# Kernel optimization log

Hardware: AMD Instinct MI355X
Metric: run time of the kernel (lower is better)

The kernel has to match this reference:

```python
import jax, jax.numpy as jnp
import numpy as np

D = 768; NH = 12; HD = D // NH; L = 12; NC = 27; PATCH = 16; MLP = 3072; PROJ = 512
IMG = 224; GRID = IMG // PATCH; HW = GRID * GRID; S = NC + HW
NEG = -1e9

def _ln(x, w, b):
    m = jnp.mean(x, -1, keepdims=True)
    v = jnp.mean(jnp.square(x - m), -1, keepdims=True)
    return (x - m) * jax.lax.rsqrt(v + 1e-5) * w + b

def _quick_gelu(x):
    return x * jax.nn.sigmoid(1.702 * x)

def _build_mask(attn_obj_masks, dtype):
    # CRIS block mask: cls<->cls blocked except self; cls->patch allowed only for
    # patches of that class; patch->cls blocked; patch->patch fully allowed.
    B = attn_obj_masks.shape[0]
    oh = jax.nn.one_hot(attn_obj_masks, NC, dtype=dtype)              # [B, HW, NC]
    T11 = jnp.broadcast_to(1.0 - jnp.eye(NC, dtype=dtype), (B, NC, NC))
    M13 = 1.0 - jnp.swapaxes(oh, 1, 2)                                # [B, NC, HW]
    top = jnp.concatenate([T11, M13], axis=2)
    bot = jnp.concatenate([jnp.ones((B, HW, NC), dtype), jnp.zeros((B, HW, HW), dtype)], axis=2)
    Mb = jnp.concatenate([top, bot], axis=1)                          # [B, S, S]
    return jnp.where(Mb == 1.0, jnp.asarray(NEG, dtype), jnp.asarray(0.0, dtype))

def reference(img, sents, attn_obj_masks, obj_masks, cls_tokens, patch_w, patch_b, pos_embed,
              ln1_w, ln1_b, qkv_w, qkv_b, out_w, out_b, ln2_w, ln2_b,
              mlp_w1, mlp_b1, mlp_w2, mlp_b2, ln_post_w, ln_post_b, proj):
    B = img.shape[0]
    sents = sents / jnp.linalg.norm(sents, axis=-1, keepdims=True)    # encode_text output, L2 normed
    mask = _build_mask(attn_obj_masks, img.dtype)                     # [B, S, S]
    # patch embedding (conv stride 16) -> [B, HW, D]
    p = jax.lax.conv_general_dilated(img, patch_w, (PATCH, PATCH), 'VALID',
                                     dimension_numbers=('NCHW', 'OIHW', 'NCHW'))
    p = p.reshape(B, D, HW).transpose(0, 2, 1) + patch_b
    x = jnp.concatenate([jnp.broadcast_to(cls_tokens, (B, NC, D)), p], axis=1) + pos_embed
    scale = 1.0 / np.sqrt(HD).astype(np.float32)
    def block(x, prm):
        l1w, l1b, qw, qb, ow, ob, l2w, l2b, w1, b1, w2, b2 = prm
        h = _ln(x, l1w, l1b)
        qkv = h @ qw + qb
        q, k, v = jnp.split(qkv, 3, axis=-1)
        q = q.reshape(B, S, NH, HD).transpose(0, 2, 1, 3)
        k = k.reshape(B, S, NH, HD).transpose(0, 2, 1, 3)
        v = v.reshape(B, S, NH, HD).transpose(0, 2, 1, 3)
        scores = jnp.einsum('bhqd,bhkd->bhqk', q, k) * scale + mask[:, None]
        a = jax.nn.softmax(scores, axis=-1)
        o = jnp.einsum('bhqk,bhkd->bhqd', a, v).transpose(0, 2, 1, 3).reshape(B, S, D)
        x = x + o @ ow + ob
        h = _ln(x, l2w, l2b)
        x = x + _quick_gelu(h @ w1 + b1) @ w2 + b2
        return x, None
    x, _ = jax.lax.scan(block, x, (ln1_w, ln1_b, qkv_w, qkv_b, out_w, out_b,
                                   ln2_w, ln2_b, mlp_w1, mlp_b1, mlp_w2, mlp_b2))
    tokens = _ln(x, ln_post_w, ln_post_b) @ proj                      # [B, S, PROJ]
    obj = tokens[:, :NC]
    obj = obj / jnp.linalg.norm(obj, axis=-1, keepdims=True)
    pred_id = jnp.einsum('bnd,bd->bn', obj, sents)                    # [B, NC]
    # per-class scatter loop == gather of pred_id by per-pixel class id
    pred = jnp.take_along_axis(pred_id, obj_masks.reshape(B, -1), axis=1).reshape(obj_masks.shape)
    return pred                                                       # [B, 224, 224]

def setup_inputs():
    B = 16; std = 0.02
    ks = jax.random.split(jax.random.key(0), 16)
    f = jax.random.normal
    return {
        'img': f(ks[0], (B, 3, IMG, IMG), jnp.float32),
        'sents': f(ks[1], (B, PROJ), jnp.float32),
        'attn_obj_masks': jax.random.randint(ks[2], (B, HW), 0, NC, jnp.int32),
        'obj_masks': jax.random.randint(ks[3], (B, IMG, IMG), 0, NC, jnp.int32),
        'cls_tokens': f(ks[4], (1, NC, D)) * std,
        'patch_w': f(ks[5], (D, 3, PATCH, PATCH)) * std,
        'patch_b': jnp.zeros((D,)),
        'pos_embed': f(ks[6], (S, D)) * std,
        'ln1_w': jnp.ones((L, D)), 'ln1_b': jnp.zeros((L, D)),
        'qkv_w': f(ks[7], (L, D, 3 * D)) * std, 'qkv_b': jnp.zeros((L, 3 * D)),
        'out_w': f(ks[8], (L, D, D)) * std, 'out_b': jnp.zeros((L, D)),
        'ln2_w': jnp.ones((L, D)), 'ln2_b': jnp.zeros((L, D)),
        'mlp_w1': f(ks[9], (L, D, MLP)) * std, 'mlp_b1': jnp.zeros((L, MLP)),
        'mlp_w2': f(ks[10], (L, MLP, D)) * std, 'mlp_b2': jnp.zeros((L, D)),
        'ln_post_w': jnp.ones((D,)), 'ln_post_b': jnp.zeros((D,)),
        'proj': f(ks[11], (D, PROJ)) * std,
    }
```

## Files before the change

kernel.cpp:

```cpp
#include <hip/hip_runtime.h>

#define DEV __device__ __forceinline__

typedef short bf16x8 __attribute__((ext_vector_type(8)));
typedef float f32x4 __attribute__((ext_vector_type(4)));
typedef int vi4 __attribute__((ext_vector_type(4)));
typedef unsigned uint2v __attribute__((ext_vector_type(2)));
typedef unsigned short u16;
typedef short short4v __attribute__((ext_vector_type(4)));

#define NEGV -1000000000.0f

DEV u16 f2bf(float f) {
  union { float f; unsigned u; } v; v.f = f;
  unsigned r = v.u + 0x7FFFu + ((v.u >> 16) & 1u);
  return (u16)(r >> 16);
}

DEV bf16x8 ld_bf8(const u16* p) {
  vi4 v = *(const vi4*)p;
  return __builtin_bit_cast(bf16x8, v);
}

DEV void gload_lds16(const u16* g, vi4* l) {
  __builtin_amdgcn_global_load_lds((const __attribute__((address_space(1))) void*)g,
                                   (__attribute__((address_space(3))) void*)l, 16, 0, 0);
}

DEV unsigned lds_off(const void* p) {
  return (unsigned)(unsigned long long)(const __attribute__((address_space(3))) void*)p;
}

DEV uint2v ds_tr16(unsigned byteaddr) {
  uint2v r;
  asm volatile("ds_read_b64_tr_b16 %0, %1" : "=v"(r) : "v"(byteaddr));
  return r;
}

template<int BN, int MODE, bool GELU, int KS>
__global__ __launch_bounds__(256) void gemm_bt(
    const u16* __restrict__ A, const u16* __restrict__ Bt,
    const float* __restrict__ bias,
    float* __restrict__ Cf, u16* __restrict__ Cb,
    int M, int N, int K, const float* __restrict__ pos, long pstride)
{
  constexpr int FJ = BN / 32;
  constexpr int LTOT = 4 + FJ;
  __shared__ vi4 As[2][1024];
  __shared__ vi4 Bs[2][BN * 8];

  int gx = gridDim.x, gy = gridDim.y;
  int nwg = gx * gy * (int)gridDim.z;
  int orig = blockIdx.x + gx * (blockIdx.y + gy * blockIdx.z);
  int qq = nwg >> 3, rr = nwg & 7;
  int xcd = orig & 7, off = orig >> 3;
  int id = (xcd < rr) ? xcd * (qq + 1) + off : rr * (qq + 1) + (xcd - rr) * qq + off;
  int bx = id % gx, rest = id / gx, by = rest % gy, bz = rest / gy;

  int tid = threadIdx.x, lane = tid & 63, wid = tid >> 6;
  int wm = wid >> 1, wn = wid & 1;
  int m0 = by * 128, n0 = bx * BN;
  int kBeg = (K / KS) * bz;
  int nT = (K / KS) >> 6;
  f32x4 acc[4][FJ] = {};

  auto STAGE = [&](int buf, int kk) {
    #pragma unroll
    for (int r = 0; r < 4; ++r) {
      int flat = r * 256 + tid;
      int row = flat >> 3, c = flat & 7;
      int cs = c ^ (row & 7);
      gload_lds16(A + (long)(m0 + row) * K + kk + cs * 8, &As[buf][r * 256 + wid * 64]);
    }
    #pragma unroll
    for (int r = 0; r < FJ; ++r) {
      int flat = r * 256 + tid;
      int row = flat >> 3, c = flat & 7;
      int cs = c ^ (row & 7);
      gload_lds16(Bt + (long)(n0 + row) * K + kk + cs * 8, &Bs[buf][r * 256 + wid * 64]);
    }
  };

  STAGE(0, kBeg);
  int cur = 0;
  for (int t = 0; t < nT; ++t) {
    if (t + 1 < nT) {
      STAGE(cur ^ 1, kBeg + (t + 1) * 64);
      asm volatile("s_waitcnt vmcnt(%0)" :: "i"(LTOT) : "memory");
    } else {
      asm volatile("s_waitcnt vmcnt(0)" ::: "memory");
    }
    __builtin_amdgcn_s_barrier();
    int cg = lane >> 4, l15 = lane & 15;
    #pragma unroll
    for (int ks = 0; ks < 2; ++ks) {
      bf16x8 af[4], bfr[FJ];
      #pragma unroll
      for (int i = 0; i < 4; ++i) {
        int ra = wm * 64 + i * 16 + l15;
        af[i] = __builtin_bit_cast(bf16x8, As[cur][ra * 8 + ((ks * 4 + cg) ^ (ra & 7))]);
      }
      #pragma unroll
      for (int j = 0; j < FJ; ++j) {
        int rb = wn * (BN / 2) + j * 16 + l15;
        bfr[j] = __builtin_bit_cast(bf16x8, Bs[cur][rb * 8 + ((ks * 4 + cg) ^ (rb & 7))]);
      }
      #pragma unroll
      for (int i = 0; i < 4; ++i)
        #pragma unroll
        for (int j = 0; j < FJ; ++j)
          acc[i][j] = __builtin_amdgcn_mfma_f32_16x16x32_bf16(af[i], bfr[j], acc[i][j], 0, 0, 0);
    }
    __builtin_amdgcn_s_barrier();
    cur ^= 1;
  }

  int cg = lane >> 4, l15 = lane & 15;
  float* Cfz = (MODE == 2 && KS > 1) ? Cf + (long)bz * pstride : Cf;
  #pragma unroll
  for (int i = 0; i < 4; ++i) {
    #pragma unroll
    for (int j = 0; j < FJ; ++j) {
      int col = n0 + wn * (BN / 2) + j * 16 + l15;
      float bv = bias ? bias[col] : 0.f;
      #pragma unroll
      for (int r = 0; r < 4; ++r) {
        int row = m0 + wm * 64 + i * 16 + cg * 4 + r;
        if (row < M) {
          float v = acc[i][j][r];
          if (KS == 1 || bz == 0) v += bv;
          if (GELU) v = v / (1.f + __expf(-1.702f * v));
          if (MODE == 0) Cb[(long)row * N + col] = f2bf(v);
          else if (MODE == 2) Cfz[(long)row * N + col] = v;
          else {
            int hw = row % 196;
            int xr = (row / 196) * 223 + 27 + hw;
            Cf[(long)xr * 768 + col] = v + pos[(27 + hw) * 768 + col];
          }
        }
      }
    }
  }
}

__global__ __launch_bounds__(256) void attn_kernel(
    const u16* __restrict__ QKV, const int* __restrict__ aom, u16* __restrict__ O)
{
  __shared__ vi4 Kl[224 * 8];
  __shared__ vi4 Vl[224 * 8];
  __shared__ int ml[196];
  int tid = threadIdx.x, lane = tid & 63, wid = tid >> 6;
  int orig = blockIdx.x + 2 * (blockIdx.y + 12 * blockIdx.z);
  int id = (orig & 7) * 48 + (orig >> 3);
  int qg = id & 1, h = (id >> 1) % 12, b = id / 24;
  long rowbase = (long)b * 223;
  #pragma unroll
  for (int it = 0; it < 7; ++it) {
    int flat = it * 256 + tid;
    int s = flat >> 3, c = flat & 7;
    int cs = c ^ (s & 7);
    gload_lds16(QKV + (rowbase + s) * 2304 + 768 + h * 64 + cs * 8, &Kl[it * 256 + wid * 64]);
  }
  #pragma unroll
  for (int it = 0; it < 7; ++it) {
    int u = it * 256 + tid;
    int slin = u >> 3, inner = u & 7;
    int sk = slin >> 2, sdp = slin & 3;
    int s = sk * 4 + (inner >> 1);
    int c = ((sdp ^ (sk & 3)) << 1) | (inner & 1);
    gload_lds16(QKV + (rowbase + s) * 2304 + 1536 + h * 64 + c * 8, &Vl[it * 256 + wid * 64]);
  }
  for (int i = tid; i < 196; i += 256) ml[i] = aom[b * 196 + i];
  __syncthreads();

  int l15 = lane & 15, cg = lane >> 4;
  unsigned vbase = lds_off(Vl);
  #pragma unroll
  for (int rep = 0; rep < 2; ++rep) {
    int fo = wid * 2 + rep;
    if (fo >= 7) break;
    int qf = qg * 7 + fo;
    int q0 = qf * 16;
    int arow = q0 + l15; if (arow > 222) arow = 222;
    const u16* qb = QKV + (rowbase + arow) * 2304 + h * 64;
    bf16x8 aq0 = ld_bf8(qb + cg * 8);
    bf16x8 aq1 = ld_bf8(qb + 32 + cg * 8);

    f32x4 sc[14];
    #pragma unroll
    for (int kf = 0; kf < 14; ++kf) {
      int key = kf * 16 + l15;
      f32x4 a = {0.f, 0.f, 0.f, 0.f};
      bf16x8 bk0 = __builtin_bit_cast(bf16x8, Kl[key * 8 + (cg ^ (key & 7))]);
      bf16x8 bk1 = __builtin_bit_cast(bf16x8, Kl[key * 8 + ((4 + cg) ^ (key & 7))]);
      a = __builtin_amdgcn_mfma_f32_16x16x32_bf16(bk0, aq0, a, 0, 0, 0);
      a = __builtin_amdgcn_mfma_f32_16x16x32_bf16(bk1, aq1, a, 0, 0, 0);
      sc[kf] = a;
    }
    int q = q0 + l15;
    float mx = -3.4e38f;
    #pragma unroll
    for (int kf = 0; kf < 14; ++kf) {
      #pragma unroll
      for (int r = 0; r < 4; ++r) {
        int key = kf * 16 + cg * 4 + r;
        float mval;
        if (key >= 223) mval = NEGV;
        else if (q >= 27) mval = (key < 27) ? NEGV : 0.f;
        else if (key < 27) mval = (key == q) ? 0.f : NEGV;
        else mval = (ml[key - 27] == q) ? 0.f : NEGV;
        float sv = sc[kf][r] * 0.125f + mval;
        sc[kf][r] = sv;
        mx = fmaxf(mx, sv);
      }
    }
    mx = fmaxf(mx, __shfl_xor(mx, 16));
    mx = fmaxf(mx, __shfl_xor(mx, 32));
    float sum = 0.f;
    #pragma unroll
    for (int kf = 0; kf < 14; ++kf) {
      #pragma unroll
      for (int r = 0; r < 4; ++r) {
        float e = __expf(sc[kf][r] - mx);
        sc[kf][r] = e; sum += e;
      }
    }
    sum += __shfl_xor(sum, 16);
    sum += __shfl_xor(sum, 32);
    float inv = 1.f / sum;
    unsigned plo[14], phi[14];
    #pragma unroll
    for (int kf = 0; kf < 14; ++kf) {
      plo[kf] = (unsigned)f2bf(sc[kf][0] * inv) | ((unsigned)f2bf(sc[kf][1] * inv) << 16);
      phi[kf] = (unsigned)f2bf(sc[kf][2] * inv) | ((unsigned)f2bf(sc[kf][3] * inv) << 16);
    }
    f32x4 oacc[4] = {};
    #pragma unroll
    for (int ks = 0; ks < 7; ++ks) {
      uint2v vr[4][2];
      int sk0 = ks * 8 + cg * 2, sk1 = sk0 + 1;
      #pragma unroll
      for (int nf = 0; nf < 4; ++nf) {
        vr[nf][0] = ds_tr16(vbase + (unsigned)(((sk0 * 4 + (nf ^ (sk0 & 3))) << 7) + l15 * 8));
        vr[nf][1] = ds_tr16(vbase + (unsigned)(((sk1 * 4 + (nf ^ (sk1 & 3))) << 7) + l15 * 8));
      }
      int src0 = ((cg & 1) << 5) + l15, src1 = src0 + 16;
      int lo0 = __shfl((int)plo[2 * ks], src0),     hi0 = __shfl((int)phi[2 * ks], src0);
      int lo1 = __shfl((int)plo[2 * ks + 1], src0), hi1 = __shfl((int)phi[2 * ks + 1], src0);
      int lo0b = __shfl((int)plo[2 * ks], src1),     hi0b = __shfl((int)phi[2 * ks], src1);
      int lo1b = __shfl((int)plo[2 * ks + 1], src1), hi1b = __shfl((int)phi[2 * ks + 1], src1);
      bool hg = (cg >> 1) & 1;
      vi4 paw = { hg ? lo1 : lo0, hg ? hi1 : hi0, hg ? lo1b : lo0b, hg ? hi1b : hi0b };
      bf16x8 pa = __builtin_bit_cast(bf16x8, paw);
      asm volatile("s_waitcnt lgkmcnt(0)" ::: "memory");
      __builtin_amdgcn_sched_barrier(0);
      #pragma unroll
      for (int nf = 0; nf < 4; ++nf) {
        vi4 bw = { (int)vr[nf][0][0], (int)vr[nf][0][1], (int)vr[nf][1][0], (int)vr[nf][1][1] };
        oacc[nf] = __builtin_amdgcn_mfma_f32_16x16x32_bf16(pa, __builtin_bit_cast(bf16x8, bw), oacc[nf], 0, 0, 0);
      }
    }
    #pragma unroll
    for (int nf = 0; nf < 4; ++nf) {
      int d = h * 64 + nf * 16 + l15;
      #pragma unroll
      for (int r = 0; r < 4; ++r) {
        int qo = q0 + cg * 4 + r;
        if (qo < 223) O[(rowbase + qo) * 768 + d] = f2bf(oacc[nf][r]);
      }
    }
  }
}

template<int NADD, bool MAP27, bool WRITEX>
__global__ __launch_bounds__(256) void ln_kernel(
    const float* __restrict__ X, const float* __restrict__ P, long ps,
    float* __restrict__ Xout, u16* __restrict__ Hb,
    const float* __restrict__ w, const float* __restrict__ bb, int nrows)
{
  int row = blockIdx.x * 4 + (threadIdx.x >> 6);
  if (row >= nrows) return;
  int xr = MAP27 ? (row / 27) * 223 + (row % 27) : row;
  int l = threadIdx.x & 63;
  const float4* xp = (const float4*)(X + (long)xr * 768);
  float4 a = xp[l], c = xp[l + 64], d = xp[l + 128];
  if (NADD == 2) {
    const float4* p0 = (const float4*)(P + (long)xr * 768);
    const float4* p1 = (const float4*)(P + ps + (long)xr * 768);
    float4 u0 = p0[l], u1 = p0[l + 64], u2 = p0[l + 128];
    float4 v0 = p1[l], v1 = p1[l + 64], v2 = p1[l + 128];
    a.x += u0.x + v0.x; a.y += u0.y + v0.y; a.z += u0.z + v0.z; a.w += u0.w + v0.w;
    c.x += u1.x + v1.x; c.y += u1.y + v1.y; c.z += u1.z + v1.z; c.w += u1.w + v1.w;
    d.x += u2.x + v2.x; d.y += u2.y + v2.y; d.z += u2.z + v2.z; d.w += u2.w + v2.w;
  }
  if (WRITEX) {
    float4* xo = (float4*)(Xout + (long)xr * 768);
    xo[l] = a; xo[l + 64] = c; xo[l + 128] = d;
  }
  float s = a.x + a.y + a.z + a.w + c.x + c.y + c.z + c.w + d.x + d.y + d.z + d.w;
  #pragma unroll
  for (int t = 1; t < 64; t <<= 1) s += __shfl_xor(s, t);
  float mean = s * (1.f / 768.f);
  a.x -= mean; a.y -= mean; a.z -= mean; a.w -= mean;
  c.x -= mean; c.y -= mean; c.z -= mean; c.w -= mean;
  d.x -= mean; d.y -= mean; d.z -= mean; d.w -= mean;
  float q = a.x*a.x + a.y*a.y + a.z*a.z + a.w*a.w
          + c.x*c.x + c.y*c.y + c.z*c.z + c.w*c.w
          + d.x*d.x + d.y*d.y + d.z*d.z + d.w*d.w;
  #pragma unroll
  for (int t = 1; t < 64; t <<= 1) q += __shfl_xor(q, t);
  float rs = rsqrtf(q * (1.f / 768.f) + 1e-5f);
  const float4* wp = (const float4*)w;
  const float4* bp = (const float4*)bb;
  u16* out = Hb + (long)row * 768;
  float4 w0 = wp[l], w1 = wp[l + 64], w2 = wp[l + 128];
  float4 b0 = bp[l], b1 = bp[l + 64], b2 = bp[l + 128];
  short4v o;
  o[0] = (short)f2bf(a.x * rs * w0.x + b0.x); o[1] = (short)f2bf(a.y * rs * w0.y + b0.y);
  o[2] = (short)f2bf(a.z * rs * w0.z + b0.z); o[3] = (short)f2bf(a.w * rs * w0.w + b0.w);
  *(short4v*)(out + l * 4) = o;
  o[0] = (short)f2bf(c.x * rs * w1.x + b1.x); o[1] = (short)f2bf(c.y * rs * w1.y + b1.y);
  o[2] = (short)f2bf(c.z * rs * w1.z + b1.z); o[3] = (short)f2bf(c.w * rs * w1.w + b1.w);
  *(short4v*)(out + 256 + l * 4) = o;
  o[0] = (short)f2bf(d.x * rs * w2.x + b2.x); o[1] = (short)f2bf(d.y * rs * w2.y + b2.y);
  o[2] = (short)f2bf(d.z * rs * w2.z + b2.z); o[3] = (short)f2bf(d.w * rs * w2.w + b2.w);
  *(short4v*)(out + 512 + l * 4) = o;
}

__global__ __launch_bounds__(256) void transpose_w(
    const float* __restrict__ W, u16* __restrict__ WT, int K, int N, long sW, long sT)
{
  __shared__ float t[64][65];
  int z = blockIdx.z;
  W += (long)z * sW; WT += (long)z * sT;
  int n0 = blockIdx.x * 64, k0 = blockIdx.y * 64;
  #pragma unroll
  for (int i = 0; i < 4; ++i) {
    int flat = i * 256 + threadIdx.x;
    int r = flat >> 4, c = (flat & 15) * 4;
    float4 v = *(const float4*)(W + (long)(k0 + r) * N + n0 + c);
    t[r][c] = v.x; t[r][c + 1] = v.y; t[r][c + 2] = v.z; t[r][c + 3] = v.w;
  }
  __syncthreads();
  #pragma unroll
  for (int i = 0; i < 8; ++i) {
    int flat = i * 256 + threadIdx.x;
    int rn = flat >> 5, ck = (flat & 31) * 2;
    unsigned val = (unsigned)f2bf(t[ck][rn]) | ((unsigned)f2bf(t[ck + 1][rn]) << 16);
    *(unsigned*)(WT + (long)(n0 + rn) * K + k0 + ck) = val;
  }
}

__global__ void convert_bf16(const float* __restrict__ src, u16* __restrict__ dst, int n) {
  int i = blockIdx.x * 256 + threadIdx.x;
  if (i < n) dst[i] = f2bf(src[i]);
}

__global__ __launch_bounds__(192) void patch_extract(const float* __restrict__ img, u16* __restrict__ Xp) {
  int row = blockIdx.x;
  int t = threadIdx.x;
  int pair = t >> 2, part = t & 3;
  int cch = pair >> 4, kh = pair & 15;
  int b = row / 196, hw = row % 196, gh = hw / 14, gw = hw % 14;
  float4 v = *(const float4*)(img + ((long)(b * 3 + cch) * 224 + gh * 16 + kh) * 224 + gw * 16 + part * 4);
  short4v o;
  o[0] = (short)f2bf(v.x); o[1] = (short)f2bf(v.y); o[2] = (short)f2bf(v.z); o[3] = (short)f2bf(v.w);
  *(short4v*)(Xp + (long)row * 768 + pair * 16 + part * 4) = o;
}

__global__ void cls_pos_fill(const float* __restrict__ cls, const float* __restrict__ pos, float* __restrict__ x) {
  int i = blockIdx.x * 256 + threadIdx.x;
  if (i >= 16 * 27 * 768) return;
  int d = i % 768, t = i / 768, b = t / 27, s = t % 27;
  x[((long)b * 223 + s) * 768 + d] = cls[s * 768 + d] + pos[s * 768 + d];
}

__global__ __launch_bounds__(256) void sents_norm(const float* __restrict__ s, float* __restrict__ sn) {
  __shared__ float sb[4];
  int b = blockIdx.x, t = threadIdx.x;
  float v0 = s[b * 512 + t], v1 = s[b * 512 + t + 256];
  float q = v0 * v0 + v1 * v1;
  #pragma unroll
  for (int d = 1; d < 64; d <<= 1) q += __shfl_xor(q, d);
  if ((t & 63) == 0) sb[t >> 6] = q;
  __syncthreads();
  float inv = rsqrtf(sb[0] + sb[1] + sb[2] + sb[3]);
  sn[b * 512 + t] = v0 * inv;
  sn[b * 512 + t + 256] = v1 * inv;
}

__global__ __launch_bounds__(256) void obj_dot(const float* __restrict__ obj, const float* __restrict__ sn, float* __restrict__ pid) {
  __shared__ float sb[8];
  int r = blockIdx.x, t = threadIdx.x, b = r / 27;
  float v0 = obj[(long)r * 512 + t], v1 = obj[(long)r * 512 + t + 256];
  float w0 = sn[b * 512 + t], w1 = sn[b * 512 + t + 256];
  float q = v0 * v0 + v1 * v1;
  float dt = v0 * w0 + v1 * w1;
  #pragma unroll
  for (int d = 1; d < 64; d <<= 1) { q += __shfl_xor(q, d); dt += __shfl_xor(dt, d); }
  if ((t & 63) == 0) { sb[t >> 6] = q; sb[4 + (t >> 6)] = dt; }
  __syncthreads();
  if (t == 0) pid[r] = (sb[4] + sb[5] + sb[6] + sb[7]) * rsqrtf(sb[0] + sb[1] + sb[2] + sb[3]);
}

__global__ void gather_pred(const int* __restrict__ om, const float* __restrict__ pid, float* __restrict__ out) {
  int i = blockIdx.x * 256 + threadIdx.x;
  if (i >= 16 * 224 * 224) return;
  int b = i / (224 * 224);
  out[i] = pid[b * 27 + om[i]];
}

extern "C" void kernel_launch(void* const* d_in, const int* in_sizes, int n_in,
                              void* d_out, int out_size, void* d_ws, size_t ws_size,
                              hipStream_t stream) {
  const float* img     = (const float*)d_in[0];
  const float* sents   = (const float*)d_in[1];
  const int*   aom     = (const int*)d_in[2];
  const int*   omask   = (const int*)d_in[3];
  const float* cls     = (const float*)d_in[4];
  const float* patch_w = (const float*)d_in[5];
  const float* patch_b = (const float*)d_in[6];
  const float* pos     = (const float*)d_in[7];
  const float* ln1w    = (const float*)d_in[8];
  const float* ln1b    = (const float*)d_in[9];
  const float* qkvw    = (const float*)d_in[10];
  const float* qkvb    = (const float*)d_in[11];
  const float* outw    = (const float*)d_in[12];
  const float* outb    = (const float*)d_in[13];
  const float* ln2w    = (const float*)d_in[14];
  const float* ln2b    = (const float*)d_in[15];
  const float* m1w     = (const float*)d_in[16];
  const float* m1b     = (const float*)d_in[17];
  const float* m2w     = (const float*)d_in[18];
  const float* m2b     = (const float*)d_in[19];
  const float* lnpw    = (const float*)d_in[20];
  const float* lnpb    = (const float*)d_in[21];
  const float* projw   = (const float*)d_in[22];

  char* p = (char*)d_ws;
  auto alloc = [&](size_t bytes) { char* r = p; p += (bytes + 255) & ~(size_t)255; return r; };
  const long PS = 3584l * 768;
  float* x   = (float*)alloc(3568ul * 768 * 4);
  u16* H     = (u16*)alloc(3584ul * 768 * 2);
  u16* QKV   = (u16*)alloc(3584ul * 2304 * 2);
  u16* Obuf  = (u16*)alloc(3584ul * 768 * 2);
  u16* G     = (u16*)alloc(3584ul * 3072 * 2);
  float* Y   = (float*)alloc((size_t)PS * 2 * 4);
  float* Mp  = (float*)alloc((size_t)PS * 2 * 4);
  u16* PWc   = (u16*)alloc(768ul * 768 * 2);
  u16* PrT   = (u16*)alloc(512ul * 768 * 2);
  float* obj = (float*)alloc(432ul * 512 * 4);
  float* sn  = (float*)alloc(16ul * 512 * 4);
  float* pid = (float*)alloc(432ul * 4);

  const size_t wlayer = (2304ul * 768 + 768ul * 768 + 3072ul * 768 + 768ul * 3072) * 2;
  size_t used = (size_t)(p - (char*)d_ws);
  int nw = (ws_size >= used + 12 * wlayer + 65536) ? 12 : 1;
  const long sQ = 2304l * 768, sO = 768l * 768, s1 = 768l * 3072, s2 = 3072l * 768;
  u16* WqT = (u16*)alloc((size_t)sQ * 2 * nw);
  u16* WoT = (u16*)alloc((size_t)sO * 2 * nw);
  u16* W1T = (u16*)alloc((size_t)s1 * 2 * nw);
  u16* W2T = (u16*)alloc((size_t)s2 * 2 * nw);

  convert_bf16<<<2304, 256, 0, stream>>>(patch_w, PWc, 768 * 768);
  transpose_w<<<dim3(8, 12, 1), 256, 0, stream>>>(projw, PrT, 768, 512, 0, 0);
  if (nw == 12) {
    transpose_w<<<dim3(36, 12, 12), 256, 0, stream>>>(qkvw, WqT, 768, 2304, sQ, sQ);
    transpose_w<<<dim3(12, 12, 12), 256, 0, stream>>>(outw, WoT, 768, 768, sO, sO);
    transpose_w<<<dim3(48, 12, 12), 256, 0, stream>>>(m1w, W1T, 768, 3072, s1, s1);
    transpose_w<<<dim3(12, 48, 12), 256, 0, stream>>>(m2w, W2T, 3072, 768, s2, s2);
  }
  patch_extract<<<3136, 192, 0, stream>>>(img, H);
  cls_pos_fill<<<1296, 256, 0, stream>>>(cls, pos, x);
  gemm_bt<64, 3, false, 1><<<dim3(12, 25), 256, 0, stream>>>(H, PWc, patch_b, x, nullptr, 3136, 768, 768, pos, 0);

  for (int l = 0; l < 12; ++l) {
    u16 *wq, *wo, *w1, *w2;
    if (nw == 12) { wq = WqT + (long)l * sQ; wo = WoT + (long)l * sO; w1 = W1T + (long)l * s1; w2 = W2T + (long)l * s2; }
    else {
      wq = WqT; wo = WoT; w1 = W1T; w2 = W2T;
      transpose_w<<<dim3(36, 12, 1), 256, 0, stream>>>(qkvw + (long)l * sQ, wq, 768, 2304, 0, 0);
      transpose_w<<<dim3(12, 12, 1), 256, 0, stream>>>(outw + (long)l * sO, wo, 768, 768, 0, 0);
      transpose_w<<<dim3(48, 12, 1), 256, 0, stream>>>(m1w + (long)l * s1, w1, 768, 3072, 0, 0);
      transpose_w<<<dim3(12, 48, 1), 256, 0, stream>>>(m2w + (long)l * s2, w2, 3072, 768, 0, 0);
    }
    if (l == 0)
      ln_kernel<0, false, false><<<892, 256, 0, stream>>>(x, nullptr, 0, nullptr, H, ln1w, ln1b, 3568);
    else
      ln_kernel<2, false, true><<<892, 256, 0, stream>>>(x, Mp, PS, x, H, ln1w + l * 768, ln1b + l * 768, 3568);
    gemm_bt<128, 0, false, 1><<<dim3(18, 28), 256, 0, stream>>>(H, wq, qkvb + l * 2304, nullptr, QKV, 3568, 2304, 768, nullptr, 0);
    attn_kernel<<<dim3(2, 12, 16), 256, 0, stream>>>(QKV, aom, Obuf);
    gemm_bt<64, 2, false, 2><<<dim3(12, 28, 2), 256, 0, stream>>>(Obuf, wo, outb + l * 768, Y, nullptr, 3568, 768, 768, nullptr, PS);
    ln_kernel<2, false, true><<<892, 256, 0, stream>>>(x, Y, PS, x, H, ln2w + l * 768, ln2b + l * 768, 3568);
    gemm_bt<128, 0, true, 1><<<dim3(24, 28), 256, 0, stream>>>(H, w1, m1b + l * 3072, nullptr, G, 3568, 3072, 768, nullptr, 0);
    gemm_bt<64, 2, false, 2><<<dim3(12, 28, 2), 256, 0, stream>>>(G, w2, m2b + l * 768, Mp, nullptr, 3568, 768, 3072, nullptr, PS);
  }

  ln_kernel<2, true, false><<<108, 256, 0, stream>>>(x, Mp, PS, nullptr, H, lnpw, lnpb, 432);
  gemm_bt<64, 2, false, 1><<<dim3(8, 4), 256, 0, stream>>>(H, PrT, nullptr, obj, nullptr, 432, 512, 768, nullptr, 0);
  sents_norm<<<16, 256, 0, stream>>>(sents, sn);
  obj_dot<<<432, 256, 0, stream>>>(obj, sn, pid);
  gather_pred<<<3136, 256, 0, stream>>>(omask, pid, (float*)d_out);
}
```

Baseline: 2.139 ms.

## Prefetch Q fragments before barrier, vectorize convert, fuse tail kernels, split-K projection

In attention, Q fragments are now loaded into registers before the LDS barrier so their global latency overlaps the K/V staging. The patch weight conversion kernel now processes four floats per thread. The final projection GEMM uses split-K into two partial buffers, and the sentence normalization is fused into the object dot kernel, which also sums the partials, removing one launch. These are small tail-end savings. The prefetch holds more live registers in the attention kernel.

```diff
diff --git a/kernel.cpp b/kernel.cpp
--- a/kernel.cpp
+++ b/kernel.cpp
@@ -171,9 +171,20 @@
     gload_lds16(QKV + (rowbase + s) * 2304 + 1536 + h * 64 + c * 8, &Vl[it * 256 + wid * 64]);
   }
   for (int i = tid; i < 196; i += 256) ml[i] = aom[b * 196 + i];
+
+  int l15 = lane & 15, cg = lane >> 4;
+  bf16x8 aq[2][2];
+  #pragma unroll
+  for (int rep = 0; rep < 2; ++rep) {
+    int fo = wid * 2 + rep;
+    int qf = qg * 7 + (fo < 7 ? fo : 6);
+    int arow = qf * 16 + l15; if (arow > 222) arow = 222;
+    const u16* qb = QKV + (rowbase + arow) * 2304 + h * 64;
+    aq[rep][0] = ld_bf8(qb + cg * 8);
+    aq[rep][1] = ld_bf8(qb + 32 + cg * 8);
+  }
   __syncthreads();
 
-  int l15 = lane & 15, cg = lane >> 4;
   unsigned vbase = lds_off(Vl);
   #pragma unroll
   for (int rep = 0; rep < 2; ++rep) {
@@ -181,10 +192,6 @@
     if (fo >= 7) break;
     int qf = qg * 7 + fo;
     int q0 = qf * 16;
-    int arow = q0 + l15; if (arow > 222) arow = 222;
-    const u16* qb = QKV + (rowbase + arow) * 2304 + h * 64;
-    bf16x8 aq0 = ld_bf8(qb + cg * 8);
-    bf16x8 aq1 = ld_bf8(qb + 32 + cg * 8);
 
     f32x4 sc[14];
     #pragma unroll
@@ -193,8 +200,8 @@
       f32x4 a = {0.f, 0.f, 0.f, 0.f};
       bf16x8 bk0 = __builtin_bit_cast(bf16x8, Kl[key * 8 + (cg ^ (key & 7))]);
       bf16x8 bk1 = __builtin_bit_cast(bf16x8, Kl[key * 8 + ((4 + cg) ^ (key & 7))]);
-      a = __builtin_amdgcn_mfma_f32_16x16x32_bf16(bk0, aq0, a, 0, 0, 0);
-      a = __builtin_amdgcn_mfma_f32_16x16x32_bf16(bk1, aq1, a, 0, 0, 0);
+      a = __builtin_amdgcn_mfma_f32_16x16x32_bf16(bk0, aq[rep][0], a, 0, 0, 0);
+      a = __builtin_amdgcn_mfma_f32_16x16x32_bf16(bk1, aq[rep][1], a, 0, 0, 0);
       sc[kf] = a;
     }
     int q = q0 + l15;
@@ -351,9 +358,14 @@
   }
 }
 
-__global__ void convert_bf16(const float* __restrict__ src, u16* __restrict__ dst, int n) {
+__global__ void convert_bf16(const float* __restrict__ src, u16* __restrict__ dst, int n4) {
   int i = blockIdx.x * 256 + threadIdx.x;
-  if (i < n) dst[i] = f2bf(src[i]);
+  if (i < n4) {
+    float4 v = ((const float4*)src)[i];
+    short4v o;
+    o[0] = (short)f2bf(v.x); o[1] = (short)f2bf(v.y); o[2] = (short)f2bf(v.z); o[3] = (short)f2bf(v.w);
+    *(short4v*)(dst + i * 4) = o;
+  }
 }
 
 __global__ __launch_bounds__(192) void patch_extract(const float* __restrict__ img, u16* __restrict__ Xp) {
@@ -375,32 +387,29 @@
   x[((long)b * 223 + s) * 768 + d] = cls[s * 768 + d] + pos[s * 768 + d];
 }
 
-__global__ __launch_bounds__(256) void sents_norm(const float* __restrict__ s, float* __restrict__ sn) {
-  __shared__ float sb[4];
-  int b = blockIdx.x, t = threadIdx.x;
-  float v0 = s[b * 512 + t], v1 = s[b * 512 + t + 256];
-  float q = v0 * v0 + v1 * v1;
-  #pragma unroll
-  for (int d = 1; d < 64; d <<= 1) q += __shfl_xor(q, d);
-  if ((t & 63) == 0) sb[t >> 6] = q;
-  __syncthreads();
-  float inv = rsqrtf(sb[0] + sb[1] + sb[2] + sb[3]);
-  sn[b * 512 + t] = v0 * inv;
-  sn[b * 512 + t + 256] = v1 * inv;
-}
-
-__global__ __launch_bounds__(256) void obj_dot(const float* __restrict__ obj, const float* __restrict__ sn, float* __restrict__ pid) {
-  __shared__ float sb[8];
+__global__ __launch_bounds__(256) void norm_dot(
+    const float* __restrict__ objp, long ps, const float* __restrict__ sents,
+    float* __restrict__ pid)
+{
+  __shared__ float sb[12];
   int r = blockIdx.x, t = threadIdx.x, b = r / 27;
-  float v0 = obj[(long)r * 512 + t], v1 = obj[(long)r * 512 + t + 256];
-  float w0 = sn[b * 512 + t], w1 = sn[b * 512 + t + 256];
+  long base = (long)r * 512;
+  float v0 = objp[base + t] + objp[ps + base + t];
+  float v1 = objp[base + t + 256] + objp[ps + base + t + 256];
+  float w0 = sents[b * 512 + t], w1 = sents[b * 512 + t + 256];
   float q = v0 * v0 + v1 * v1;
   float dt = v0 * w0 + v1 * w1;
-  #pragma unroll
-  for (int d = 1; d < 64; d <<= 1) { q += __shfl_xor(q, d); dt += __shfl_xor(dt, d); }
-  if ((t & 63) == 0) { sb[t >> 6] = q; sb[4 + (t >> 6)] = dt; }
+  float sw = w0 * w0 + w1 * w1;
+  #pragma unroll
+  for (int d = 1; d < 64; d <<= 1) {
+    q += __shfl_xor(q, d); dt += __shfl_xor(dt, d); sw += __shfl_xor(sw, d);
+  }
+  if ((t & 63) == 0) { sb[t >> 6] = q; sb[4 + (t >> 6)] = dt; sb[8 + (t >> 6)] = sw; }
   __syncthreads();
-  if (t == 0) pid[r] = (sb[4] + sb[5] + sb[6] + sb[7]) * rsqrtf(sb[0] + sb[1] + sb[2] + sb[3]);
+  if (t == 0)
+    pid[r] = (sb[4] + sb[5] + sb[6] + sb[7])
+           * rsqrtf(sb[0] + sb[1] + sb[2] + sb[3])
+           * rsqrtf(sb[8] + sb[9] + sb[10] + sb[11]);
 }
 
 __global__ void gather_pred(const int* __restrict__ om, const float* __restrict__ pid, float* __restrict__ out) {
@@ -440,6 +449,7 @@
   char* p = (char*)d_ws;
   auto alloc = [&](size_t bytes) { char* r = p; p += (bytes + 255) & ~(size_t)255; return r; };
   const long PS = 3584l * 768;
+  const long OPS = 432l * 512;
   float* x   = (float*)alloc(3568ul * 768 * 4);
   u16* H     = (u16*)alloc(3584ul * 768 * 2);
   u16* QKV   = (u16*)alloc(3584ul * 2304 * 2);
@@ -449,8 +459,7 @@
   float* Mp  = (float*)alloc((size_t)PS * 2 * 4);
   u16* PWc   = (u16*)alloc(768ul * 768 * 2);
   u16* PrT   = (u16*)alloc(512ul * 768 * 2);
-  float* obj = (float*)alloc(432ul * 512 * 4);
-  float* sn  = (float*)alloc(16ul * 512 * 4);
+  float* obj = (float*)alloc((size_t)OPS * 2 * 4);
   float* pid = (float*)alloc(432ul * 4);
 
   const size_t wlayer = (2304ul * 768 + 768ul * 768 + 3072ul * 768 + 768ul * 3072) * 2;
@@ -462,7 +471,7 @@
   u16* W1T = (u16*)alloc((size_t)s1 * 2 * nw);
   u16* W2T = (u16*)alloc((size_t)s2 * 2 * nw);
 
-  convert_bf16<<<2304, 256, 0, stream>>>(patch_w, PWc, 768 * 768);
+  convert_bf16<<<576, 256, 0, stream>>>(patch_w, PWc, 147456);
   transpose_w<<<dim3(8, 12, 1), 256, 0, stream>>>(projw, PrT, 768, 512, 0, 0);
   if (nw == 12) {
     transpose_w<<<dim3(36, 12, 12), 256, 0, stream>>>(qkvw, WqT, 768, 2304, sQ, sQ);
@@ -497,8 +506,7 @@
   }
 
   ln_kernel<2, true, false><<<108, 256, 0, stream>>>(x, Mp, PS, nullptr, H, lnpw, lnpb, 432);
-  gemm_bt<64, 2, false, 1><<<dim3(8, 4), 256, 0, stream>>>(H, PrT, nullptr, obj, nullptr, 432, 512, 768, nullptr, 0);
-  sents_norm<<<16, 256, 0, stream>>>(sents, sn);
-  obj_dot<<<432, 256, 0, stream>>>(obj, sn, pid);
+  gemm_bt<64, 2, false, 2><<<dim3(8, 4, 2), 256, 0, stream>>>(H, PrT, nullptr, obj, nullptr, 432, 512, 768, nullptr, OPS);
+  norm_dot<<<432, 256, 0, stream>>>(obj, OPS, sents, pid);
   gather_pred<<<3136, 256, 0, stream>>>(omask, pid, (float*)d_out);
 }
```

Result: no change. 2.138 ms (-0.0%).
